# Optimization experiments

Hardware: AMD Instinct MI355X
Metric: run time of the kernel (lower is better)

Reference implementation:

```python
import jax, jax.numpy as jnp
import numpy as np

N = 2048

def setup_inputs() -> dict:
    key = jax.random.key(0)
    k0, k1, k2, k3 = jax.random.split(key, 4)
    return {
        "input": jax.random.normal(k0, (N, N), dtype=jnp.float32),
        "weight1": jax.random.normal(k1, (N, N), dtype=jnp.float32),
        "weight2": jax.random.normal(k2, (N, N), dtype=jnp.float32),
        "weight3": jax.random.normal(k3, (N, N), dtype=jnp.float32),
    }

def reference(input, weight1, weight2, weight3):
    # Faithful translation of the torch DAG (duplicate mm kept: t4 == t2,
    # so t8 is mathematically zero, but we preserve the original math).
    t1 = input @ weight1
    t2 = input @ weight2
    t3 = weight3 @ weight3
    t4 = input @ weight2
    t5 = t1 * weight1
    t6 = (t5 @ input) * weight1
    t7 = t1 * t2 + t1 + t3
    t8 = t2 - t4
    t9 = t7 * t8 + t6 * t3
    t11 = t3 * t9
    t12 = t3 * (t1 @ input) * t6
    t13 = t7 + t11
    t14 = t8 + t12
    t15 = t13 + t14
    return t15
```

## Files before the change

kernel.cpp:

```cpp
#include <hip/hip_runtime.h>
#include <hip/hip_bf16.h>
#include <stdint.h>

#define NN 2048
#define BM 128
#define BN 128
#define BK 32

typedef __bf16 bf16;
typedef __bf16 bf16x8 __attribute__((ext_vector_type(8)));
typedef __bf16 bf16x4 __attribute__((ext_vector_type(4)));
typedef float f32x4 __attribute__((ext_vector_type(4)));

__device__ __forceinline__ void async_copy16(bf16* lds, const bf16* g) {
    __builtin_amdgcn_global_load_lds(
        (const __attribute__((address_space(1))) unsigned int*)g,
        (__attribute__((address_space(3))) unsigned int*)lds,
        16, 0, 0);
}

#define WAIT_VM8() asm volatile("s_waitcnt vmcnt(8)" ::: "memory")
#define WAIT_VM4() asm volatile("s_waitcnt vmcnt(4)" ::: "memory")
#define WAIT_VM0() asm volatile("s_waitcnt vmcnt(0)" ::: "memory")
#define BAR()                                  \
    do {                                       \
        asm volatile("" ::: "memory");         \
        __builtin_amdgcn_s_barrier();          \
        asm volatile("" ::: "memory");         \
    } while (0)

struct CastArgs {
    const float* in[4];
    bf16*        outT[4];
    bf16*        outN[4];
};

__global__ __launch_bounds__(256) void transpose_cast_kernel(CastArgs args) {
    const float* __restrict__ in = args.in[blockIdx.z];
    bf16* __restrict__ outT      = args.outT[blockIdx.z];
    bf16* __restrict__ outN      = args.outN[blockIdx.z];
    __shared__ float tile[64][65];
    const int bx = blockIdx.x * 64;
    const int by = blockIdx.y * 64;
    const int t  = threadIdx.x;
    const int tc = t & 15, tr = t >> 4;
#pragma unroll
    for (int p = 0; p < 4; ++p) {
        const int r = tr + p * 16;
        const float4 v = *(const float4*)&in[(size_t)(by + r) * NN + bx + tc * 4];
        tile[r][tc * 4 + 0] = v.x; tile[r][tc * 4 + 1] = v.y;
        tile[r][tc * 4 + 2] = v.z; tile[r][tc * 4 + 3] = v.w;
        if (outN) {
            bf16x4 b = {(bf16)v.x, (bf16)v.y, (bf16)v.z, (bf16)v.w};
            *(bf16x4*)&outN[(size_t)(by + r) * NN + bx + tc * 4] = b;
        }
    }
    __syncthreads();
    const int cc = t >> 2, e = t & 3;
#pragma unroll
    for (int u = 0; u < 2; ++u) {
        const int r0 = e * 16 + u * 8;
        bf16x8 b;
#pragma unroll
        for (int i = 0; i < 8; ++i) b[i] = (bf16)tile[r0 + i][cc];
        *(bf16x8*)&outT[(size_t)(bx + cc) * NN + by + r0] = b;
    }
}

struct GemmArgs {
    const bf16* A[3];
    const bf16* Bt[3];
    float*      C[3];
};

__global__ __launch_bounds__(256) void gemm_bt_batched(GemmArgs args) {
    const bf16* __restrict__ A  = args.A[blockIdx.z];
    const bf16* __restrict__ Bt = args.Bt[blockIdx.z];
    float* __restrict__ C       = args.C[blockIdx.z];

    __shared__ bf16 As0[BM * BK], As1[BM * BK], As2[BM * BK];
    __shared__ bf16 Bs0[BN * BK], Bs1[BN * BK], Bs2[BN * BK];

    const int t  = threadIdx.x;
    const int bm = blockIdx.x * BM;
    const int bn = blockIdx.y * BN;

    const int row0 = t >> 2;
    const int qp   = t & 3;
    const int col0 = ((qp ^ ((row0 >> 1) & 3)) << 3);
    const int off0 = t * 8;

    const bf16* gA0 = A  + (size_t)(bm + row0) * NN + col0;
    const bf16* gB0 = Bt + (size_t)(bn + row0) * NN + col0;

    const int wave = t >> 6;
    const int lane = t & 63;
    const int wm   = (wave >> 1) * 64;
    const int wn   = (wave & 1) * 64;
    const int lrow = lane & 15;
    const int q    = lane >> 4;
    const int qe   = (q ^ ((lrow >> 1) & 3)) << 3;

    f32x4 acc[4][4];
#pragma unroll
    for (int i = 0; i < 4; ++i)
#pragma unroll
        for (int j = 0; j < 4; ++j) acc[i][j] = (f32x4){0.f, 0.f, 0.f, 0.f};

    auto issue = [&](bf16* As, bf16* Bs, int kt) {
        const int kof = kt * BK;
        async_copy16(&As[off0],           gA0 + kof);
        async_copy16(&As[off0 + 64 * BK], gA0 + (size_t)64 * NN + kof);
        async_copy16(&Bs[off0],           gB0 + kof);
        async_copy16(&Bs[off0 + 64 * BK], gB0 + (size_t)64 * NN + kof);
    };
    auto compute = [&](const bf16* As, const bf16* Bs) {
        bf16x8 af[4], bfr[4];
#pragma unroll
        for (int i = 0; i < 4; ++i)
            af[i] = *(const bf16x8*)&As[(wm + i * 16 + lrow) * BK + qe];
#pragma unroll
        for (int j = 0; j < 4; ++j)
            bfr[j] = *(const bf16x8*)&Bs[(wn + j * 16 + lrow) * BK + qe];
#pragma unroll
        for (int i = 0; i < 4; ++i)
#pragma unroll
            for (int j = 0; j < 4; ++j)
                acc[i][j] = __builtin_amdgcn_mfma_f32_16x16x32_bf16(
                    af[i], bfr[j], acc[i][j], 0, 0, 0);
    };

    issue(As0, Bs0, 0);
    issue(As1, Bs1, 1);

#pragma unroll 1
    for (int kt = 0; kt < 60; kt += 3) {
        issue(As2, Bs2, kt + 2); WAIT_VM8(); BAR(); compute(As0, Bs0); BAR();
        issue(As0, Bs0, kt + 3); WAIT_VM8(); BAR(); compute(As1, Bs1); BAR();
        issue(As1, Bs1, kt + 4); WAIT_VM8(); BAR(); compute(As2, Bs2); BAR();
    }
    issue(As2, Bs2, 62); WAIT_VM8(); BAR(); compute(As0, Bs0); BAR();
    issue(As0, Bs0, 63); WAIT_VM8(); BAR(); compute(As1, Bs1); BAR();
    WAIT_VM4(); BAR(); compute(As2, Bs2); BAR();
    WAIT_VM0(); BAR(); compute(As0, Bs0);

#pragma unroll
    for (int i = 0; i < 4; ++i)
#pragma unroll
        for (int j = 0; j < 4; ++j)
#pragma unroll
            for (int r = 0; r < 4; ++r)
                C[(size_t)(bm + wm + i * 16 + q * 4 + r) * NN +
                  (bn + wn + j * 16 + lrow)] = acc[i][j][r];
}

__global__ void post_m1_kernel(const float* __restrict__ M1,
                               const float* __restrict__ W1,
                               bf16* __restrict__ M1bf,
                               bf16* __restrict__ B1bf) {
    const size_t i = ((size_t)blockIdx.x * 256 + threadIdx.x) * 4;
    const float4 m = *(const float4*)&M1[i];
    const float4 w = *(const float4*)&W1[i];
    bf16x4 mb = {(bf16)m.x, (bf16)m.y, (bf16)m.z, (bf16)m.w};
    bf16x4 bb = {(bf16)(m.x * w.x), (bf16)(m.y * w.y),
                 (bf16)(m.z * w.z), (bf16)(m.w * w.w)};
    *(bf16x4*)&M1bf[i] = mb;
    *(bf16x4*)&B1bf[i] = bb;
}

__global__ void epilogue_kernel(const float* __restrict__ M1,
                                const float* __restrict__ M3,
                                const float* __restrict__ M4,
                                const float* __restrict__ M5,
                                const float* __restrict__ W1,
                                float* __restrict__ out) {
    const size_t i = ((size_t)blockIdx.x * 256 + threadIdx.x) * 4;
    const float4 m1 = *(const float4*)&M1[i];
    const float4 m3 = *(const float4*)&M3[i];
    const float4 m4 = *(const float4*)&M4[i];
    const float4 m5 = *(const float4*)&M5[i];
    const float4 w1 = *(const float4*)&W1[i];
    const float4 m2 = *(const float4*)&out[i];
    float4 r;
    r.x = m1.x * m2.x + m1.x + m3.x + m3.x * (m4.x * w1.x) * (m3.x + m5.x);
    r.y = m1.y * m2.y + m1.y + m3.y + m3.y * (m4.y * w1.y) * (m3.y + m5.y);
    r.z = m1.z * m2.z + m1.z + m3.z + m3.z * (m4.z * w1.z) * (m3.z + m5.z);
    r.w = m1.w * m2.w + m1.w + m3.w + m3.w * (m4.w * w1.w) * (m3.w + m5.w);
    *(float4*)&out[i] = r;
}

extern "C" void kernel_launch(void* const* d_in, const int* in_sizes, int n_in,
                              void* d_out, int out_size, void* d_ws, size_t ws_size,
                              hipStream_t stream) {
    const float* A  = (const float*)d_in[0];
    const float* W1 = (const float*)d_in[1];
    const float* W2 = (const float*)d_in[2];
    const float* W3 = (const float*)d_in[3];
    float* out = (float*)d_out;

    const size_t P = (size_t)NN * NN;
    char* ws = (char*)d_ws;

    bf16* Abf  = (bf16*)ws;
    bf16* At   = Abf + P;
    bf16* W1t  = At + P;
    bf16* W2t  = W1t + P;
    bf16* W3bf = W2t + P;
    bf16* W3t  = W3bf + P;
    float* M1  = (float*)(W3t + P);
    float* M3  = M1 + P;
    float* M4  = M3 + P;
    float* M5  = M4 + P;

    CastArgs ca;
    ca.in[0] = A;  ca.outT[0] = At;  ca.outN[0] = Abf;
    ca.in[1] = W1; ca.outT[1] = W1t; ca.outN[1] = nullptr;
    ca.in[2] = W2; ca.outT[2] = W2t; ca.outN[2] = nullptr;
    ca.in[3] = W3; ca.outT[3] = W3t; ca.outN[3] = W3bf;
    transpose_cast_kernel<<<dim3(NN / 64, NN / 64, 4), 256, 0, stream>>>(ca);

    GemmArgs g3;
    g3.A[0] = Abf;  g3.Bt[0] = W1t; g3.C[0] = M1;
    g3.A[1] = Abf;  g3.Bt[1] = W2t; g3.C[1] = out;
    g3.A[2] = W3bf; g3.Bt[2] = W3t; g3.C[2] = M3;
    gemm_bt_batched<<<dim3(NN / BM, NN / BN, 3), 256, 0, stream>>>(g3);

    bf16* M1bf = W2t;
    bf16* B1bf = W3bf;
    post_m1_kernel<<<(P / 4) / 256, 256, 0, stream>>>(M1, W1, M1bf, B1bf);

    GemmArgs g2;
    g2.A[0] = M1bf; g2.Bt[0] = At; g2.C[0] = M5;
    g2.A[1] = B1bf; g2.Bt[1] = At; g2.C[1] = M4;
    g2.A[2] = M1bf; g2.Bt[2] = At; g2.C[2] = M5;
    gemm_bt_batched<<<dim3(NN / BM, NN / BN, 2), 256, 0, stream>>>(g2);

    epilogue_kernel<<<(P / 4) / 256, 256, 0, stream>>>(M1, M3, M4, M5, W1, out);
}
```

Measured before the change: 237.6 us.

## Fuse elementwise post/epilogue into GEMMs and shrink tiles to 64x64

The post-M1 cast kernel is folded into the first batched GEMM's epilogue (z==0 writes the bf16 M1 and M1*W1 copies). The final elementwise kernel is fused into a second GEMM that computes M5 and M4 together, sharing the At tile. Tiles shrink from 128x128 to 64x64 so each wave does a 32x32 sub-tile. This removes two launches and the M4/M5 round trips through memory. In exchange it lowers arithmetic intensity and MFMA reuse per LDS load, and the fused epilogue does scattered scalar global reads.

```diff
diff --git a/kernel.cpp b/kernel.cpp
--- a/kernel.cpp
+++ b/kernel.cpp
@@ -3,8 +3,6 @@
 #include <stdint.h>
 
 #define NN 2048
-#define BM 128
-#define BN 128
 #define BK 32
 
 typedef __bf16 bf16;
@@ -19,9 +17,7 @@
         16, 0, 0);
 }
 
-#define WAIT_VM8() asm volatile("s_waitcnt vmcnt(8)" ::: "memory")
-#define WAIT_VM4() asm volatile("s_waitcnt vmcnt(4)" ::: "memory")
-#define WAIT_VM0() asm volatile("s_waitcnt vmcnt(0)" ::: "memory")
+#define WAIT_VM(n) asm volatile("s_waitcnt vmcnt(" #n ")" ::: "memory")
 #define BAR()                                  \
     do {                                       \
         asm volatile("" ::: "memory");         \
@@ -67,23 +63,26 @@
     }
 }
 
-struct GemmArgs {
-    const bf16* A[3];
-    const bf16* Bt[3];
-    float*      C[3];
+struct Gemm3Args {
+    const bf16*  A[3];
+    const bf16*  Bt[3];
+    float*       C[3];
+    const float* W1;
+    bf16*        M1bf;
+    bf16*        B1bf;
 };
 
-__global__ __launch_bounds__(256) void gemm_bt_batched(GemmArgs args) {
+__global__ __launch_bounds__(256) void gemm3_kernel(Gemm3Args args) {
     const bf16* __restrict__ A  = args.A[blockIdx.z];
     const bf16* __restrict__ Bt = args.Bt[blockIdx.z];
     float* __restrict__ C       = args.C[blockIdx.z];
 
-    __shared__ bf16 As0[BM * BK], As1[BM * BK], As2[BM * BK];
-    __shared__ bf16 Bs0[BN * BK], Bs1[BN * BK], Bs2[BN * BK];
+    __shared__ bf16 As0[64 * BK], As1[64 * BK], As2[64 * BK];
+    __shared__ bf16 Bs0[64 * BK], Bs1[64 * BK], Bs2[64 * BK];
 
     const int t  = threadIdx.x;
-    const int bm = blockIdx.x * BM;
-    const int bn = blockIdx.y * BN;
+    const int bm = blockIdx.x * 64;
+    const int bn = blockIdx.y * 64;
 
     const int row0 = t >> 2;
     const int qp   = t & 3;
@@ -95,98 +94,173 @@
 
     const int wave = t >> 6;
     const int lane = t & 63;
-    const int wm   = (wave >> 1) * 64;
-    const int wn   = (wave & 1) * 64;
+    const int wm   = (wave >> 1) * 32;
+    const int wn   = (wave & 1) * 32;
     const int lrow = lane & 15;
     const int q    = lane >> 4;
     const int qe   = (q ^ ((lrow >> 1) & 3)) << 3;
 
-    f32x4 acc[4][4];
-#pragma unroll
-    for (int i = 0; i < 4; ++i)
-#pragma unroll
-        for (int j = 0; j < 4; ++j) acc[i][j] = (f32x4){0.f, 0.f, 0.f, 0.f};
+    f32x4 acc[2][2];
+#pragma unroll
+    for (int i = 0; i < 2; ++i)
+#pragma unroll
+        for (int j = 0; j < 2; ++j) acc[i][j] = (f32x4){0.f, 0.f, 0.f, 0.f};
 
     auto issue = [&](bf16* As, bf16* Bs, int kt) {
         const int kof = kt * BK;
-        async_copy16(&As[off0],           gA0 + kof);
-        async_copy16(&As[off0 + 64 * BK], gA0 + (size_t)64 * NN + kof);
-        async_copy16(&Bs[off0],           gB0 + kof);
-        async_copy16(&Bs[off0 + 64 * BK], gB0 + (size_t)64 * NN + kof);
+        async_copy16(&As[off0], gA0 + kof);
+        async_copy16(&Bs[off0], gB0 + kof);
     };
     auto compute = [&](const bf16* As, const bf16* Bs) {
-        bf16x8 af[4], bfr[4];
-#pragma unroll
-        for (int i = 0; i < 4; ++i)
+        bf16x8 af[2], bfr[2];
+#pragma unroll
+        for (int i = 0; i < 2; ++i)
             af[i] = *(const bf16x8*)&As[(wm + i * 16 + lrow) * BK + qe];
 #pragma unroll
-        for (int j = 0; j < 4; ++j)
+        for (int j = 0; j < 2; ++j)
             bfr[j] = *(const bf16x8*)&Bs[(wn + j * 16 + lrow) * BK + qe];
 #pragma unroll
-        for (int i = 0; i < 4; ++i)
-#pragma unroll
-            for (int j = 0; j < 4; ++j)
+        for (int i = 0; i < 2; ++i)
+#pragma unroll
+            for (int j = 0; j < 2; ++j)
                 acc[i][j] = __builtin_amdgcn_mfma_f32_16x16x32_bf16(
                     af[i], bfr[j], acc[i][j], 0, 0, 0);
     };
 
     issue(As0, Bs0, 0);
     issue(As1, Bs1, 1);
-
 #pragma unroll 1
     for (int kt = 0; kt < 60; kt += 3) {
-        issue(As2, Bs2, kt + 2); WAIT_VM8(); BAR(); compute(As0, Bs0); BAR();
-        issue(As0, Bs0, kt + 3); WAIT_VM8(); BAR(); compute(As1, Bs1); BAR();
-        issue(As1, Bs1, kt + 4); WAIT_VM8(); BAR(); compute(As2, Bs2); BAR();
+        issue(As2, Bs2, kt + 2); WAIT_VM(4); BAR(); compute(As0, Bs0); BAR();
+        issue(As0, Bs0, kt + 3); WAIT_VM(4); BAR(); compute(As1, Bs1); BAR();
+        issue(As1, Bs1, kt + 4); WAIT_VM(4); BAR(); compute(As2, Bs2); BAR();
     }
-    issue(As2, Bs2, 62); WAIT_VM8(); BAR(); compute(As0, Bs0); BAR();
-    issue(As0, Bs0, 63); WAIT_VM8(); BAR(); compute(As1, Bs1); BAR();
-    WAIT_VM4(); BAR(); compute(As2, Bs2); BAR();
-    WAIT_VM0(); BAR(); compute(As0, Bs0);
-
-#pragma unroll
-    for (int i = 0; i < 4; ++i)
-#pragma unroll
-        for (int j = 0; j < 4; ++j)
-#pragma unroll
-            for (int r = 0; r < 4; ++r)
-                C[(size_t)(bm + wm + i * 16 + q * 4 + r) * NN +
-                  (bn + wn + j * 16 + lrow)] = acc[i][j][r];
-}
-
-__global__ void post_m1_kernel(const float* __restrict__ M1,
-                               const float* __restrict__ W1,
-                               bf16* __restrict__ M1bf,
-                               bf16* __restrict__ B1bf) {
-    const size_t i = ((size_t)blockIdx.x * 256 + threadIdx.x) * 4;
-    const float4 m = *(const float4*)&M1[i];
-    const float4 w = *(const float4*)&W1[i];
-    bf16x4 mb = {(bf16)m.x, (bf16)m.y, (bf16)m.z, (bf16)m.w};
-    bf16x4 bb = {(bf16)(m.x * w.x), (bf16)(m.y * w.y),
-                 (bf16)(m.z * w.z), (bf16)(m.w * w.w)};
-    *(bf16x4*)&M1bf[i] = mb;
-    *(bf16x4*)&B1bf[i] = bb;
-}
-
-__global__ void epilogue_kernel(const float* __restrict__ M1,
-                                const float* __restrict__ M3,
-                                const float* __restrict__ M4,
-                                const float* __restrict__ M5,
-                                const float* __restrict__ W1,
-                                float* __restrict__ out) {
-    const size_t i = ((size_t)blockIdx.x * 256 + threadIdx.x) * 4;
-    const float4 m1 = *(const float4*)&M1[i];
-    const float4 m3 = *(const float4*)&M3[i];
-    const float4 m4 = *(const float4*)&M4[i];
-    const float4 m5 = *(const float4*)&M5[i];
-    const float4 w1 = *(const float4*)&W1[i];
-    const float4 m2 = *(const float4*)&out[i];
-    float4 r;
-    r.x = m1.x * m2.x + m1.x + m3.x + m3.x * (m4.x * w1.x) * (m3.x + m5.x);
-    r.y = m1.y * m2.y + m1.y + m3.y + m3.y * (m4.y * w1.y) * (m3.y + m5.y);
-    r.z = m1.z * m2.z + m1.z + m3.z + m3.z * (m4.z * w1.z) * (m3.z + m5.z);
-    r.w = m1.w * m2.w + m1.w + m3.w + m3.w * (m4.w * w1.w) * (m3.w + m5.w);
-    *(float4*)&out[i] = r;
+    issue(As2, Bs2, 62); WAIT_VM(4); BAR(); compute(As0, Bs0); BAR();
+    issue(As0, Bs0, 63); WAIT_VM(4); BAR(); compute(As1, Bs1); BAR();
+    WAIT_VM(2); BAR(); compute(As2, Bs2); BAR();
+    WAIT_VM(0); BAR(); compute(As0, Bs0);
+
+    const int z = blockIdx.z;
+#pragma unroll
+    for (int i = 0; i < 2; ++i)
+#pragma unroll
+        for (int j = 0; j < 2; ++j)
+#pragma unroll
+            for (int r = 0; r < 4; ++r) {
+                const size_t idx = (size_t)(bm + wm + i * 16 + q * 4 + r) * NN +
+                                   (bn + wn + j * 16 + lrow);
+                const float v = acc[i][j][r];
+                C[idx] = v;
+                if (z == 0) {
+                    const float w = args.W1[idx];
+                    args.M1bf[idx] = (bf16)v;
+                    args.B1bf[idx] = (bf16)(v * w);
+                }
+            }
+}
+
+struct Gemm2Args {
+    const bf16*  M1bf;
+    const bf16*  B1bf;
+    const bf16*  At;
+    const float* M1;
+    const float* M3;
+    const float* W1;
+    float*       out;
+};
+
+__global__ __launch_bounds__(256) void gemm2_fused_kernel(Gemm2Args args) {
+    __shared__ bf16 A50[64 * BK], A51[64 * BK], A52[64 * BK];
+    __shared__ bf16 A40[64 * BK], A41[64 * BK], A42[64 * BK];
+    __shared__ bf16 Bs0[64 * BK], Bs1[64 * BK], Bs2[64 * BK];
+
+    const int t  = threadIdx.x;
+    const int bm = blockIdx.x * 64;
+    const int bn = blockIdx.y * 64;
+
+    const int row0 = t >> 2;
+    const int qp   = t & 3;
+    const int col0 = ((qp ^ ((row0 >> 1) & 3)) << 3);
+    const int off0 = t * 8;
+
+    const bf16* g5 = args.M1bf + (size_t)(bm + row0) * NN + col0;
+    const bf16* g4 = args.B1bf + (size_t)(bm + row0) * NN + col0;
+    const bf16* gB = args.At   + (size_t)(bn + row0) * NN + col0;
+
+    const int wave = t >> 6;
+    const int lane = t & 63;
+    const int wm   = (wave >> 1) * 32;
+    const int wn   = (wave & 1) * 32;
+    const int lrow = lane & 15;
+    const int q    = lane >> 4;
+    const int qe   = (q ^ ((lrow >> 1) & 3)) << 3;
+
+    f32x4 acc5[2][2], acc4[2][2];
+#pragma unroll
+    for (int i = 0; i < 2; ++i)
+#pragma unroll
+        for (int j = 0; j < 2; ++j) {
+            acc5[i][j] = (f32x4){0.f, 0.f, 0.f, 0.f};
+            acc4[i][j] = (f32x4){0.f, 0.f, 0.f, 0.f};
+        }
+
+    auto issue = [&](bf16* A5, bf16* A4, bf16* Bs, int kt) {
+        const int kof = kt * BK;
+        async_copy16(&A5[off0], g5 + kof);
+        async_copy16(&A4[off0], g4 + kof);
+        async_copy16(&Bs[off0], gB + kof);
+    };
+    auto compute = [&](const bf16* A5, const bf16* A4, const bf16* Bs) {
+        bf16x8 a5[2], a4[2], bfr[2];
+#pragma unroll
+        for (int i = 0; i < 2; ++i) {
+            a5[i] = *(const bf16x8*)&A5[(wm + i * 16 + lrow) * BK + qe];
+            a4[i] = *(const bf16x8*)&A4[(wm + i * 16 + lrow) * BK + qe];
+        }
+#pragma unroll
+        for (int j = 0; j < 2; ++j)
+            bfr[j] = *(const bf16x8*)&Bs[(wn + j * 16 + lrow) * BK + qe];
+#pragma unroll
+        for (int i = 0; i < 2; ++i)
+#pragma unroll
+            for (int j = 0; j < 2; ++j) {
+                acc5[i][j] = __builtin_amdgcn_mfma_f32_16x16x32_bf16(
+                    a5[i], bfr[j], acc5[i][j], 0, 0, 0);
+                acc4[i][j] = __builtin_amdgcn_mfma_f32_16x16x32_bf16(
+                    a4[i], bfr[j], acc4[i][j], 0, 0, 0);
+            }
+    };
+
+    issue(A50, A40, Bs0, 0);
+    issue(A51, A41, Bs1, 1);
+#pragma unroll 1
+    for (int kt = 0; kt < 60; kt += 3) {
+        issue(A52, A42, Bs2, kt + 2); WAIT_VM(6); BAR(); compute(A50, A40, Bs0); BAR();
+        issue(A50, A40, Bs0, kt + 3); WAIT_VM(6); BAR(); compute(A51, A41, Bs1); BAR();
+        issue(A51, A41, Bs1, kt + 4); WAIT_VM(6); BAR(); compute(A52, A42, Bs2); BAR();
+    }
+    issue(A52, A42, Bs2, 62); WAIT_VM(6); BAR(); compute(A50, A40, Bs0); BAR();
+    issue(A50, A40, Bs0, 63); WAIT_VM(6); BAR(); compute(A51, A41, Bs1); BAR();
+    WAIT_VM(3); BAR(); compute(A52, A42, Bs2); BAR();
+    WAIT_VM(0); BAR(); compute(A50, A40, Bs0);
+
+#pragma unroll
+    for (int i = 0; i < 2; ++i)
+#pragma unroll
+        for (int j = 0; j < 2; ++j)
+#pragma unroll
+            for (int r = 0; r < 4; ++r) {
+                const size_t idx = (size_t)(bm + wm + i * 16 + q * 4 + r) * NN +
+                                   (bn + wn + j * 16 + lrow);
+                const float m5 = acc5[i][j][r];
+                const float m4 = acc4[i][j][r];
+                const float m1 = args.M1[idx];
+                const float m3 = args.M3[idx];
+                const float w1 = args.W1[idx];
+                const float m2 = args.out[idx];
+                args.out[idx] =
+                    m1 * m2 + m1 + m3 + m3 * (m4 * w1) * (m3 + m5);
+            }
 }
 
 extern "C" void kernel_launch(void* const* d_in, const int* in_sizes, int n_in,
@@ -207,10 +281,10 @@
     bf16* W2t  = W1t + P;
     bf16* W3bf = W2t + P;
     bf16* W3t  = W3bf + P;
-    float* M1  = (float*)(W3t + P);
+    bf16* M1bf = W3t + P;
+    bf16* B1bf = M1bf + P;
+    float* M1  = (float*)(B1bf + P);
     float* M3  = M1 + P;
-    float* M4  = M3 + P;
-    float* M5  = M4 + P;
 
     CastArgs ca;
     ca.in[0] = A;  ca.outT[0] = At;  ca.outN[0] = Abf;
@@ -219,21 +293,15 @@
     ca.in[3] = W3; ca.outT[3] = W3t; ca.outN[3] = W3bf;
     transpose_cast_kernel<<<dim3(NN / 64, NN / 64, 4), 256, 0, stream>>>(ca);
 
-    GemmArgs g3;
+    Gemm3Args g3;
     g3.A[0] = Abf;  g3.Bt[0] = W1t; g3.C[0] = M1;
     g3.A[1] = Abf;  g3.Bt[1] = W2t; g3.C[1] = out;
     g3.A[2] = W3bf; g3.Bt[2] = W3t; g3.C[2] = M3;
-    gemm_bt_batched<<<dim3(NN / BM, NN / BN, 3), 256, 0, stream>>>(g3);
-
-    bf16* M1bf = W2t;
-    bf16* B1bf = W3bf;
-    post_m1_kernel<<<(P / 4) / 256, 256, 0, stream>>>(M1, W1, M1bf, B1bf);
-
-    GemmArgs g2;
-    g2.A[0] = M1bf; g2.Bt[0] = At; g2.C[0] = M5;
-    g2.A[1] = B1bf; g2.Bt[1] = At; g2.C[1] = M4;
-    g2.A[2] = M1bf; g2.Bt[2] = At; g2.C[2] = M5;
-    gemm_bt_batched<<<dim3(NN / BM, NN / BN, 2), 256, 0, stream>>>(g2);
-
-    epilogue_kernel<<<(P / 4) / 256, 256, 0, stream>>>(M1, M3, M4, M5, W1, out);
-}
+    g3.W1 = W1; g3.M1bf = M1bf; g3.B1bf = B1bf;
+    gemm3_kernel<<<dim3(NN / 64, NN / 64, 3), 256, 0, stream>>>(g3);
+
+    Gemm2Args g2;
+    g2.M1bf = M1bf; g2.B1bf = B1bf; g2.At = At;
+    g2.M1 = M1; g2.M3 = M3; g2.W1 = W1; g2.out = out;
+    gemm2_fused_kernel<<<dim3(NN / 64, NN / 64), 256, 0, stream>>>(g2);
+}
```

New measurement: 294.3 us. 23.9% more time.
